# Kernel tuning notes

Measured on AMD Instinct MI355X. Metric: run time of the kernel, lower is better.

The kernel has to match this reference:

```python
import jax, jax.numpy as jnp
import numpy as np


def setup_inputs() -> dict:
    key = jax.random.key(0)
    k1, k2, k3 = jax.random.split(key, 3)
    B, M, T, D = 512, 4096, 48, 2
    preds = jax.random.normal(k1, (B, M), dtype=jnp.float32)
    target = jax.random.normal(k2, (B, 1, T, D), dtype=jnp.float32)
    memory = jax.random.normal(k3, (M, T, D), dtype=jnp.float32)
    return {"preds": preds, "target": target, "memory": memory}


def reference(preds, target, memory):
    # preds: [B, M]; target: [B, 1, T, D]; memory: [M, T, D]
    gt = target[:, 0]                                  # [B, T, D]
    diff = memory[None, :, :, :] - gt[:, None, :, :]   # [B, M, T, D]
    # mean over timesteps of per-timestep euclidean distance
    dist = jnp.sqrt(jnp.sum(diff * diff, axis=-1)).mean(axis=-1)  # [B, M]
    true_index = jnp.argmin(dist, axis=1)              # [B] int labels
    # cross-entropy of preds vs. nearest-mode labels, averaged over batch
    logp = jax.nn.log_softmax(preds, axis=1)           # [B, M]
    nll = -jnp.take_along_axis(logp, true_index[:, None], axis=1)[:, 0]  # [B]
    loss = nll.mean()
    return loss, true_index.astype(jnp.float32)
```

## Files before the change

kernel.cpp:

```cpp
#include <hip/hip_runtime.h>
#include <math.h>

#define B 512
#define M 4096
#define T 48
#define MCHUNK 8
#define NCH (M / MCHUNK)


__global__ __launch_bounds__(256) void k_transpose(const float* __restrict__ target,
                                                   float2* __restrict__ tgtT) {
    int i = blockIdx.x * 256 + threadIdx.x;
    int b = i / T, t = i - b * T;
    float2 v = ((const float2*)target)[i];
    tgtT[t * B + b] = v;
}

__global__ __launch_bounds__(256, 4) void k_dist(const float2* __restrict__ tgtT,
                                                 const float* __restrict__ memory,
                                                 unsigned long long* __restrict__ pval,
                                                 float* __restrict__ out0) {
    const int tid = threadIdx.x;
    const int b   = blockIdx.y * 256 + tid;
    const int ch  = blockIdx.x;
    const int m0  = ch * MCHUNK;

    if (ch == 0 && blockIdx.y == 0 && tid == 0) out0[0] = 0.0f;

    float acc[MCHUNK];
#pragma unroll
    for (int i = 0; i < MCHUNK; ++i) acc[i] = 0.f;

    for (int q = 0; q < T / 2; ++q) {
        float2 g0 = tgtT[(2 * q)     * B + b];
        float2 g1 = tgtT[(2 * q + 1) * B + b];
#pragma unroll
        for (int mi = 0; mi < MCHUNK; ++mi) {
            const float4* mr = (const float4*)(memory + (size_t)(m0 + mi) * (T * 2));
            float4 mv = mr[q];
            float dx0 = mv.x - g0.x, dy0 = mv.y - g0.y;
            float dx1 = mv.z - g1.x, dy1 = mv.w - g1.y;
            acc[mi] += __builtin_amdgcn_sqrtf(fmaf(dx0, dx0, dy0 * dy0));
            acc[mi] += __builtin_amdgcn_sqrtf(fmaf(dx1, dx1, dy1 * dy1));
        }
    }

    float bestv = INFINITY;
    int   besti = 0;
#pragma unroll
    for (int mi = 0; mi < MCHUNK; ++mi)
        if (acc[mi] < bestv) { bestv = acc[mi]; besti = m0 + mi; }

    pval[(size_t)b * NCH + ch] =
        ((unsigned long long)__float_as_uint(bestv) << 32) | (unsigned int)besti;
}

__global__ __launch_bounds__(256) void k_post(const float* __restrict__ preds,
                                              const unsigned long long* __restrict__ pval,
                                              float* __restrict__ out) {
    const int b   = blockIdx.x;
    const int tid = threadIdx.x;

    __shared__ unsigned long long sm[256];
    __shared__ float red[256];

    unsigned long long p0 = pval[(size_t)b * NCH + tid];
    unsigned long long p1 = pval[(size_t)b * NCH + 256 + tid];
    sm[tid] = p0 < p1 ? p0 : p1;
    __syncthreads();
    for (int s = 128; s > 0; s >>= 1) {
        if (tid < s) { unsigned long long o = sm[tid + s]; if (o < sm[tid]) sm[tid] = o; }
        __syncthreads();
    }
    const int idx = (int)(unsigned int)(sm[0] & 0xFFFFFFFFULL);
    __syncthreads();

    const float4* row = (const float4*)(preds + (size_t)b * M);
    float4 v[4];
    float mx = -INFINITY;
#pragma unroll
    for (int j = 0; j < 4; ++j) {
        v[j] = row[tid + j * 256];
        mx = fmaxf(mx, fmaxf(fmaxf(v[j].x, v[j].y), fmaxf(v[j].z, v[j].w)));
    }
    red[tid] = mx; __syncthreads();
    for (int s = 128; s > 0; s >>= 1) {
        if (tid < s) red[tid] = fmaxf(red[tid], red[tid + s]);
        __syncthreads();
    }
    mx = red[0];
    __syncthreads();

    float sum = 0.f;
#pragma unroll
    for (int j = 0; j < 4; ++j)
        sum += expf(v[j].x - mx) + expf(v[j].y - mx) + expf(v[j].z - mx) + expf(v[j].w - mx);
    red[tid] = sum; __syncthreads();
    for (int s = 128; s > 0; s >>= 1) {
        if (tid < s) red[tid] += red[tid + s];
        __syncthreads();
    }

    if (tid == 0) {
        float lse = mx + logf(red[0]);
        float nll = lse - preds[(size_t)b * M + idx];
        atomicAdd(out, nll * (1.0f / B));
        out[1 + b] = (float)idx;
    }
}

extern "C" void kernel_launch(void* const* d_in, const int* in_sizes, int n_in,
                              void* d_out, int out_size, void* d_ws, size_t ws_size,
                              hipStream_t stream) {
    const float* preds  = (const float*)d_in[0];
    const float* target = (const float*)d_in[1];
    const float* memory = (const float*)d_in[2];
    float* out = (float*)d_out;

    char* ws = (char*)d_ws;
    unsigned long long* pval = (unsigned long long*)ws;
    float2* tgtT = (float2*)(ws + (size_t)2 * 1024 * 1024);

    k_transpose<<<(B * T) / 256, 256, 0, stream>>>(target, tgtT);
    dim3 g1(NCH, B / 256);
    k_dist<<<g1, 256, 0, stream>>>(tgtT, memory, pval, out);
    k_post<<<B, 256, 0, stream>>>(preds, pval, out);
}
```

Baseline: 44.27 us.

## Stage memory rows in LDS, halve M chunk, warp-per-row post reduction

The distance kernel now handles 4 memory modes per block instead of 8, loads those modes' trajectories into shared memory once, and reads targets packed as float4 pairs of timesteps. Occupancy is raised through launch bounds. The post kernel gives each wavefront one batch row and reduces with shuffles instead of shared-memory tree reductions, and zeroing the loss moves into the prep kernel. The smaller chunk doubles the partial-argmin buffer and the number of blocks, which adds global write traffic and more work in the post reduction.

Result: slower. 47.11 us (+6.4%).

```diff
diff --git a/kernel.cpp b/kernel.cpp
--- a/kernel.cpp
+++ b/kernel.cpp
@@ -4,52 +4,72 @@
 #define B 512
 #define M 4096
 #define T 48
-#define MCHUNK 8
+#define MCHUNK 4
 #define NCH (M / MCHUNK)
 
 
-__global__ __launch_bounds__(256) void k_transpose(const float* __restrict__ target,
-                                                   float2* __restrict__ tgtT) {
+__global__ __launch_bounds__(256) void k_prep(const float* __restrict__ target,
+                                              float4* __restrict__ tgtP,
+                                              float* __restrict__ out0) {
     int i = blockIdx.x * 256 + threadIdx.x;
-    int b = i / T, t = i - b * T;
-    float2 v = ((const float2*)target)[i];
-    tgtT[t * B + b] = v;
+    if (i == 0) out0[0] = 0.0f;
+    int b = i / (T / 2), q = i - b * (T / 2);
+    float4 v = *(const float4*)(target + (size_t)b * (T * 2) + 4 * q);
+    tgtP[q * B + b] = v;
 }
 
-__global__ __launch_bounds__(256, 4) void k_dist(const float2* __restrict__ tgtT,
+__global__ __launch_bounds__(256, 8) void k_dist(const float4* __restrict__ tgtP,
                                                  const float* __restrict__ memory,
-                                                 unsigned long long* __restrict__ pval,
-                                                 float* __restrict__ out0) {
+                                                 unsigned long long* __restrict__ pval) {
     const int tid = threadIdx.x;
+    const int ch  = blockIdx.x;
     const int b   = blockIdx.y * 256 + tid;
-    const int ch  = blockIdx.x;
     const int m0  = ch * MCHUNK;
 
-    if (ch == 0 && blockIdx.y == 0 && tid == 0) out0[0] = 0.0f;
+    __shared__ float4 smem[MCHUNK * (T / 2)];
+    if (tid < MCHUNK * (T / 2))
+        smem[tid] = ((const float4*)(memory + (size_t)m0 * (T * 2)))[tid];
+    __syncthreads();
 
-    float acc[MCHUNK];
-#pragma unroll
-    for (int i = 0; i < MCHUNK; ++i) acc[i] = 0.f;
+    float acc0 = 0.f, acc1 = 0.f, acc2 = 0.f, acc3 = 0.f;
 
+#pragma unroll 6
     for (int q = 0; q < T / 2; ++q) {
-        float2 g0 = tgtT[(2 * q)     * B + b];
-        float2 g1 = tgtT[(2 * q + 1) * B + b];
-#pragma unroll
-        for (int mi = 0; mi < MCHUNK; ++mi) {
-            const float4* mr = (const float4*)(memory + (size_t)(m0 + mi) * (T * 2));
-            float4 mv = mr[q];
-            float dx0 = mv.x - g0.x, dy0 = mv.y - g0.y;
-            float dx1 = mv.z - g1.x, dy1 = mv.w - g1.y;
-            acc[mi] += __builtin_amdgcn_sqrtf(fmaf(dx0, dx0, dy0 * dy0));
-            acc[mi] += __builtin_amdgcn_sqrtf(fmaf(dx1, dx1, dy1 * dy1));
+        float4 g = tgtP[q * B + b];
+        {
+            float4 mv = smem[0 * (T / 2) + q];
+            float dx0 = mv.x - g.x, dy0 = mv.y - g.y;
+            float dx1 = mv.z - g.z, dy1 = mv.w - g.w;
+            acc0 += __builtin_amdgcn_sqrtf(fmaf(dx0, dx0, dy0 * dy0));
+            acc0 += __builtin_amdgcn_sqrtf(fmaf(dx1, dx1, dy1 * dy1));
+        }
+        {
+            float4 mv = smem[1 * (T / 2) + q];
+            float dx0 = mv.x - g.x, dy0 = mv.y - g.y;
+            float dx1 = mv.z - g.z, dy1 = mv.w - g.w;
+            acc1 += __builtin_amdgcn_sqrtf(fmaf(dx0, dx0, dy0 * dy0));
+            acc1 += __builtin_amdgcn_sqrtf(fmaf(dx1, dx1, dy1 * dy1));
+        }
+        {
+            float4 mv = smem[2 * (T / 2) + q];
+            float dx0 = mv.x - g.x, dy0 = mv.y - g.y;
+            float dx1 = mv.z - g.z, dy1 = mv.w - g.w;
+            acc2 += __builtin_amdgcn_sqrtf(fmaf(dx0, dx0, dy0 * dy0));
+            acc2 += __builtin_amdgcn_sqrtf(fmaf(dx1, dx1, dy1 * dy1));
+        }
+        {
+            float4 mv = smem[3 * (T / 2) + q];
+            float dx0 = mv.x - g.x, dy0 = mv.y - g.y;
+            float dx1 = mv.z - g.z, dy1 = mv.w - g.w;
+            acc3 += __builtin_amdgcn_sqrtf(fmaf(dx0, dx0, dy0 * dy0));
+            acc3 += __builtin_amdgcn_sqrtf(fmaf(dx1, dx1, dy1 * dy1));
         }
     }
 
-    float bestv = INFINITY;
-    int   besti = 0;
-#pragma unroll
-    for (int mi = 0; mi < MCHUNK; ++mi)
-        if (acc[mi] < bestv) { bestv = acc[mi]; besti = m0 + mi; }
+    float bestv = acc0; int besti = m0;
+    if (acc1 < bestv) { bestv = acc1; besti = m0 + 1; }
+    if (acc2 < bestv) { bestv = acc2; besti = m0 + 2; }
+    if (acc3 < bestv) { bestv = acc3; besti = m0 + 3; }
 
     pval[(size_t)b * NCH + ch] =
         ((unsigned long long)__float_as_uint(bestv) << 32) | (unsigned int)besti;
@@ -58,51 +78,45 @@
 __global__ __launch_bounds__(256) void k_post(const float* __restrict__ preds,
                                               const unsigned long long* __restrict__ pval,
                                               float* __restrict__ out) {
-    const int b   = blockIdx.x;
-    const int tid = threadIdx.x;
+    const int lane = threadIdx.x & 63;
+    const int wv   = threadIdx.x >> 6;
+    const int b    = blockIdx.x * 4 + wv;
 
-    __shared__ unsigned long long sm[256];
-    __shared__ float red[256];
-
-    unsigned long long p0 = pval[(size_t)b * NCH + tid];
-    unsigned long long p1 = pval[(size_t)b * NCH + 256 + tid];
-    sm[tid] = p0 < p1 ? p0 : p1;
-    __syncthreads();
-    for (int s = 128; s > 0; s >>= 1) {
-        if (tid < s) { unsigned long long o = sm[tid + s]; if (o < sm[tid]) sm[tid] = o; }
-        __syncthreads();
+    unsigned long long best = 0xFFFFFFFFFFFFFFFFULL;
+#pragma unroll
+    for (int j = 0; j < NCH / 64; ++j) {
+        unsigned long long p = pval[(size_t)b * NCH + j * 64 + lane];
+        if (p < best) best = p;
     }
-    const int idx = (int)(unsigned int)(sm[0] & 0xFFFFFFFFULL);
-    __syncthreads();
+#pragma unroll
+    for (int s = 32; s > 0; s >>= 1) {
+        unsigned long long o = __shfl_down(best, s);
+        if (o < best) best = o;
+    }
+    best = __shfl(best, 0);
+    const int idx = (int)(unsigned int)(best & 0xFFFFFFFFULL);
 
     const float4* row = (const float4*)(preds + (size_t)b * M);
-    float4 v[4];
+    float4 v[16];
     float mx = -INFINITY;
 #pragma unroll
-    for (int j = 0; j < 4; ++j) {
-        v[j] = row[tid + j * 256];
+    for (int j = 0; j < 16; ++j) {
+        v[j] = row[j * 64 + lane];
         mx = fmaxf(mx, fmaxf(fmaxf(v[j].x, v[j].y), fmaxf(v[j].z, v[j].w)));
     }
-    red[tid] = mx; __syncthreads();
-    for (int s = 128; s > 0; s >>= 1) {
-        if (tid < s) red[tid] = fmaxf(red[tid], red[tid + s]);
-        __syncthreads();
-    }
-    mx = red[0];
-    __syncthreads();
+#pragma unroll
+    for (int s = 32; s > 0; s >>= 1) mx = fmaxf(mx, __shfl_down(mx, s));
+    mx = __shfl(mx, 0);
 
     float sum = 0.f;
 #pragma unroll
-    for (int j = 0; j < 4; ++j)
+    for (int j = 0; j < 16; ++j)
         sum += expf(v[j].x - mx) + expf(v[j].y - mx) + expf(v[j].z - mx) + expf(v[j].w - mx);
-    red[tid] = sum; __syncthreads();
-    for (int s = 128; s > 0; s >>= 1) {
-        if (tid < s) red[tid] += red[tid + s];
-        __syncthreads();
-    }
+#pragma unroll
+    for (int s = 32; s > 0; s >>= 1) sum += __shfl_down(sum, s);
 
-    if (tid == 0) {
-        float lse = mx + logf(red[0]);
+    if (lane == 0) {
+        float lse = mx + logf(sum);
         float nll = lse - preds[(size_t)b * M + idx];
         atomicAdd(out, nll * (1.0f / B));
         out[1 + b] = (float)idx;
@@ -119,10 +133,10 @@
 
     char* ws = (char*)d_ws;
     unsigned long long* pval = (unsigned long long*)ws;
-    float2* tgtT = (float2*)(ws + (size_t)2 * 1024 * 1024);
+    float4* tgtP = (float4*)(ws + (size_t)4 * 1024 * 1024);
 
-    k_transpose<<<(B * T) / 256, 256, 0, stream>>>(target, tgtT);
+    k_prep<<<(B * T / 2) / 256, 256, 0, stream>>>(target, tgtP, out);
     dim3 g1(NCH, B / 256);
-    k_dist<<<g1, 256, 0, stream>>>(tgtT, memory, pval, out);
-    k_post<<<B, 256, 0, stream>>>(preds, pval, out);
+    k_dist<<<g1, 256, 0, stream>>>(tgtP, memory, pval);
+    k_post<<<B / 4, 256, 0, stream>>>(preds, pval, out);
 }
```

## Fuse transpose, distance and softmax-loss into one cooperative kernel

Applied to the files above, without the earlier changes.

Replaces the three kernel launches with a single cooperative kernel of 512 blocks that uses grid-wide syncs between the transpose, distance and post-processing phases. Each block now caches its memory chunk in shared memory and handles all 512 batch rows, two per thread. Partial argmins are stored transposed so the post phase can read them per batch. The aim is to remove launch gaps and repeated global loads of memory, at the cost of grid-sync overhead and the occupancy limits a cooperative launch imposes.

After: 148.2 us. +234.8%, slower.

```diff
diff --git a/kernel.cpp b/kernel.cpp
--- a/kernel.cpp
+++ b/kernel.cpp
@@ -1,5 +1,9 @@
 #include <hip/hip_runtime.h>
+#include <hip/hip_cooperative_groups.h>
 #include <math.h>
+
+namespace cg = cooperative_groups;
+typedef unsigned long long u64;
 
 #define B 512
 #define M 4096
@@ -8,104 +12,118 @@
 #define NCH (M / MCHUNK)
 
 
-__global__ __launch_bounds__(256) void k_transpose(const float* __restrict__ target,
-                                                   float2* __restrict__ tgtT) {
-    int i = blockIdx.x * 256 + threadIdx.x;
-    int b = i / T, t = i - b * T;
-    float2 v = ((const float2*)target)[i];
-    tgtT[t * B + b] = v;
-}
+__global__ __launch_bounds__(256, 2) void k_fused(const float* __restrict__ preds,
+                                                  const float* __restrict__ target,
+                                                  const float* __restrict__ memory,
+                                                  float* __restrict__ out,
+                                                  u64* __restrict__ pvalT,
+                                                  float4* __restrict__ tgtP) {
+    cg::grid_group grid = cg::this_grid();
+    const int tid = threadIdx.x;
+    const int bid = blockIdx.x;
 
-__global__ __launch_bounds__(256, 4) void k_dist(const float2* __restrict__ tgtT,
-                                                 const float* __restrict__ memory,
-                                                 unsigned long long* __restrict__ pval,
-                                                 float* __restrict__ out0) {
-    const int tid = threadIdx.x;
-    const int b   = blockIdx.y * 256 + tid;
-    const int ch  = blockIdx.x;
-    const int m0  = ch * MCHUNK;
+    __shared__ float4 smem[MCHUNK * (T / 2)];
+    __shared__ u64    smu[256];
+    __shared__ float  red[256];
 
-    if (ch == 0 && blockIdx.y == 0 && tid == 0) out0[0] = 0.0f;
+    {
+        int i = bid * 256 + tid;
+        if (i < B * (T / 2)) {
+            int b = i / (T / 2), q = i - b * (T / 2);
+            float4 v = *(const float4*)(target + (size_t)b * (T * 2) + 4 * q);
+            tgtP[q * B + b] = v;
+        }
+        if (i == 0) out[0] = 0.0f;
+    }
+    grid.sync();
 
-    float acc[MCHUNK];
+    {
+        const int ch = bid;
+        const int m0 = ch * MCHUNK;
+        if (tid < MCHUNK * (T / 2))
+            smem[tid] = ((const float4*)(memory + (size_t)m0 * (T * 2)))[tid];
+        __syncthreads();
+
+        float acc0[MCHUNK], acc1[MCHUNK];
 #pragma unroll
-    for (int i = 0; i < MCHUNK; ++i) acc[i] = 0.f;
+        for (int i = 0; i < MCHUNK; ++i) { acc0[i] = 0.f; acc1[i] = 0.f; }
 
-    for (int q = 0; q < T / 2; ++q) {
-        float2 g0 = tgtT[(2 * q)     * B + b];
-        float2 g1 = tgtT[(2 * q + 1) * B + b];
+#pragma unroll 4
+        for (int q = 0; q < T / 2; ++q) {
+            float4 g0 = tgtP[q * B + tid];
+            float4 g1 = tgtP[q * B + 256 + tid];
 #pragma unroll
-        for (int mi = 0; mi < MCHUNK; ++mi) {
-            const float4* mr = (const float4*)(memory + (size_t)(m0 + mi) * (T * 2));
-            float4 mv = mr[q];
-            float dx0 = mv.x - g0.x, dy0 = mv.y - g0.y;
-            float dx1 = mv.z - g1.x, dy1 = mv.w - g1.y;
-            acc[mi] += __builtin_amdgcn_sqrtf(fmaf(dx0, dx0, dy0 * dy0));
-            acc[mi] += __builtin_amdgcn_sqrtf(fmaf(dx1, dx1, dy1 * dy1));
+            for (int mi = 0; mi < MCHUNK; ++mi) {
+                float4 mv = smem[mi * (T / 2) + q];
+                float dx, dy;
+                dx = mv.x - g0.x; dy = mv.y - g0.y;
+                acc0[mi] += __builtin_amdgcn_sqrtf(fmaf(dx, dx, dy * dy));
+                dx = mv.z - g0.z; dy = mv.w - g0.w;
+                acc0[mi] += __builtin_amdgcn_sqrtf(fmaf(dx, dx, dy * dy));
+                dx = mv.x - g1.x; dy = mv.y - g1.y;
+                acc1[mi] += __builtin_amdgcn_sqrtf(fmaf(dx, dx, dy * dy));
+                dx = mv.z - g1.z; dy = mv.w - g1.w;
+                acc1[mi] += __builtin_amdgcn_sqrtf(fmaf(dx, dx, dy * dy));
+            }
         }
+
+        float bv0 = acc0[0]; int bi0 = m0;
+        float bv1 = acc1[0]; int bi1 = m0;
+#pragma unroll
+        for (int mi = 1; mi < MCHUNK; ++mi) {
+            if (acc0[mi] < bv0) { bv0 = acc0[mi]; bi0 = m0 + mi; }
+            if (acc1[mi] < bv1) { bv1 = acc1[mi]; bi1 = m0 + mi; }
+        }
+        pvalT[(size_t)ch * B + tid]       = ((u64)__float_as_uint(bv0) << 32) | (unsigned int)bi0;
+        pvalT[(size_t)ch * B + 256 + tid] = ((u64)__float_as_uint(bv1) << 32) | (unsigned int)bi1;
     }
+    grid.sync();
 
-    float bestv = INFINITY;
-    int   besti = 0;
+    {
+        const int b = bid;
+        u64 p0 = pvalT[(size_t)tid * B + b];
+        u64 p1 = pvalT[(size_t)(tid + 256) * B + b];
+        smu[tid] = p0 < p1 ? p0 : p1;
+        __syncthreads();
+        for (int s = 128; s > 0; s >>= 1) {
+            if (tid < s) { u64 o = smu[tid + s]; if (o < smu[tid]) smu[tid] = o; }
+            __syncthreads();
+        }
+        const int idx = (int)(unsigned int)(smu[0] & 0xFFFFFFFFULL);
+        __syncthreads();
+
+        const float4* row = (const float4*)(preds + (size_t)b * M);
+        float4 v[4];
+        float mx = -INFINITY;
 #pragma unroll
-    for (int mi = 0; mi < MCHUNK; ++mi)
-        if (acc[mi] < bestv) { bestv = acc[mi]; besti = m0 + mi; }
+        for (int j = 0; j < 4; ++j) {
+            v[j] = row[tid + j * 256];
+            mx = fmaxf(mx, fmaxf(fmaxf(v[j].x, v[j].y), fmaxf(v[j].z, v[j].w)));
+        }
+        red[tid] = mx; __syncthreads();
+        for (int s = 128; s > 0; s >>= 1) {
+            if (tid < s) red[tid] = fmaxf(red[tid], red[tid + s]);
+            __syncthreads();
+        }
+        mx = red[0];
+        __syncthreads();
 
-    pval[(size_t)b * NCH + ch] =
-        ((unsigned long long)__float_as_uint(bestv) << 32) | (unsigned int)besti;
-}
+        float sum = 0.f;
+#pragma unroll
+        for (int j = 0; j < 4; ++j)
+            sum += expf(v[j].x - mx) + expf(v[j].y - mx) + expf(v[j].z - mx) + expf(v[j].w - mx);
+        red[tid] = sum; __syncthreads();
+        for (int s = 128; s > 0; s >>= 1) {
+            if (tid < s) red[tid] += red[tid + s];
+            __syncthreads();
+        }
 
-__global__ __launch_bounds__(256) void k_post(const float* __restrict__ preds,
-                                              const unsigned long long* __restrict__ pval,
-                                              float* __restrict__ out) {
-    const int b   = blockIdx.x;
-    const int tid = threadIdx.x;
-
-    __shared__ unsigned long long sm[256];
-    __shared__ float red[256];
-
-    unsigned long long p0 = pval[(size_t)b * NCH + tid];
-    unsigned long long p1 = pval[(size_t)b * NCH + 256 + tid];
-    sm[tid] = p0 < p1 ? p0 : p1;
-    __syncthreads();
-    for (int s = 128; s > 0; s >>= 1) {
-        if (tid < s) { unsigned long long o = sm[tid + s]; if (o < sm[tid]) sm[tid] = o; }
-        __syncthreads();
-    }
-    const int idx = (int)(unsigned int)(sm[0] & 0xFFFFFFFFULL);
-    __syncthreads();
-
-    const float4* row = (const float4*)(preds + (size_t)b * M);
-    float4 v[4];
-    float mx = -INFINITY;
-#pragma unroll
-    for (int j = 0; j < 4; ++j) {
-        v[j] = row[tid + j * 256];
-        mx = fmaxf(mx, fmaxf(fmaxf(v[j].x, v[j].y), fmaxf(v[j].z, v[j].w)));
-    }
-    red[tid] = mx; __syncthreads();
-    for (int s = 128; s > 0; s >>= 1) {
-        if (tid < s) red[tid] = fmaxf(red[tid], red[tid + s]);
-        __syncthreads();
-    }
-    mx = red[0];
-    __syncthreads();
-
-    float sum = 0.f;
-#pragma unroll
-    for (int j = 0; j < 4; ++j)
-        sum += expf(v[j].x - mx) + expf(v[j].y - mx) + expf(v[j].z - mx) + expf(v[j].w - mx);
-    red[tid] = sum; __syncthreads();
-    for (int s = 128; s > 0; s >>= 1) {
-        if (tid < s) red[tid] += red[tid + s];
-        __syncthreads();
-    }
-
-    if (tid == 0) {
-        float lse = mx + logf(red[0]);
-        float nll = lse - preds[(size_t)b * M + idx];
-        atomicAdd(out, nll * (1.0f / B));
-        out[1 + b] = (float)idx;
+        if (tid == 0) {
+            float lse = mx + logf(red[0]);
+            float nll = lse - preds[(size_t)b * M + idx];
+            atomicAdd(out, nll * (1.0f / B));
+            out[1 + b] = (float)idx;
+        }
     }
 }
 
@@ -118,11 +136,11 @@
     float* out = (float*)d_out;
 
     char* ws = (char*)d_ws;
-    unsigned long long* pval = (unsigned long long*)ws;
-    float2* tgtT = (float2*)(ws + (size_t)2 * 1024 * 1024);
+    u64* pvalT   = (u64*)ws;
+    float4* tgtP = (float4*)(ws + (size_t)2 * 1024 * 1024);
 
-    k_transpose<<<(B * T) / 256, 256, 0, stream>>>(target, tgtT);
-    dim3 g1(NCH, B / 256);
-    k_dist<<<g1, 256, 0, stream>>>(tgtT, memory, pval, out);
-    k_post<<<B, 256, 0, stream>>>(preds, pval, out);
+    void* args[] = {(void*)&preds, (void*)&target, (void*)&memory,
+                    (void*)&out, (void*)&pvalT, (void*)&tgtP};
+    hipLaunchCooperativeKernel((const void*)k_fused, dim3(NCH), dim3(256),
+                               args, 0, stream);
 }
```

## Transpose memory instead of target and tile batch rows in shared memory

Applied to the files above, without the earlier changes.

The distance kernel is reorganised so each thread owns one memory mode and loops over a tile of 8 batch rows kept in shared memory, reading a transposed memory array with coalesced loads. Before, each thread owned one batch row and read uniform memory rows. Per-block argmin now uses wavefront shuffles, and the post kernel reduces only 16 partials per row. This cuts the partial-result traffic and the reduction work, but adds a larger transpose of the 4096x48 memory array and shared-memory reads in the inner loop.

Result: slower. 45.28 us (+2.3%).

```diff
diff --git a/kernel.cpp b/kernel.cpp
--- a/kernel.cpp
+++ b/kernel.cpp
@@ -1,79 +1,91 @@
 #include <hip/hip_runtime.h>
 #include <math.h>
+
+typedef unsigned long long u64;
 
 #define B 512
 #define M 4096
 #define T 48
-#define MCHUNK 8
-#define NCH (M / MCHUNK)
+#define BTILE 8
+#define MBLK 256
+#define NMB (M / MBLK)
 
 
-__global__ __launch_bounds__(256) void k_transpose(const float* __restrict__ target,
-                                                   float2* __restrict__ tgtT) {
+__global__ __launch_bounds__(256) void k_trans(const float* __restrict__ memory,
+                                               float2* __restrict__ memT,
+                                               float* __restrict__ out0) {
     int i = blockIdx.x * 256 + threadIdx.x;
-    int b = i / T, t = i - b * T;
-    float2 v = ((const float2*)target)[i];
-    tgtT[t * B + b] = v;
+    if (i == 0) out0[0] = 0.0f;
+    int m = i / T, t = i - m * T;
+    memT[t * M + m] = ((const float2*)memory)[i];
 }
 
-__global__ __launch_bounds__(256, 4) void k_dist(const float2* __restrict__ tgtT,
-                                                 const float* __restrict__ memory,
-                                                 unsigned long long* __restrict__ pval,
-                                                 float* __restrict__ out0) {
+__global__ __launch_bounds__(256) void k_dist(const float* __restrict__ target,
+                                              const float2* __restrict__ memT,
+                                              u64* __restrict__ pval) {
     const int tid = threadIdx.x;
-    const int b   = blockIdx.y * 256 + tid;
-    const int ch  = blockIdx.x;
-    const int m0  = ch * MCHUNK;
+    const int m   = blockIdx.x * MBLK + tid;
+    const int b0  = blockIdx.y * BTILE;
 
-    if (ch == 0 && blockIdx.y == 0 && tid == 0) out0[0] = 0.0f;
+    __shared__ float tg[BTILE * T * 2];
+    __shared__ u64   su[4][BTILE];
 
-    float acc[MCHUNK];
+    if (tid < BTILE * T * 2 / 4)
+        ((float4*)tg)[tid] = ((const float4*)(target + (size_t)b0 * (T * 2)))[tid];
+    __syncthreads();
+
+    float acc[BTILE];
 #pragma unroll
-    for (int i = 0; i < MCHUNK; ++i) acc[i] = 0.f;
+    for (int bi = 0; bi < BTILE; ++bi) acc[bi] = 0.f;
 
-    for (int q = 0; q < T / 2; ++q) {
-        float2 g0 = tgtT[(2 * q)     * B + b];
-        float2 g1 = tgtT[(2 * q + 1) * B + b];
+#pragma unroll 2
+    for (int t = 0; t < T; ++t) {
+        float2 mv = memT[t * M + m];
 #pragma unroll
-        for (int mi = 0; mi < MCHUNK; ++mi) {
-            const float4* mr = (const float4*)(memory + (size_t)(m0 + mi) * (T * 2));
-            float4 mv = mr[q];
-            float dx0 = mv.x - g0.x, dy0 = mv.y - g0.y;
-            float dx1 = mv.z - g1.x, dy1 = mv.w - g1.y;
-            acc[mi] += __builtin_amdgcn_sqrtf(fmaf(dx0, dx0, dy0 * dy0));
-            acc[mi] += __builtin_amdgcn_sqrtf(fmaf(dx1, dx1, dy1 * dy1));
+        for (int bi = 0; bi < BTILE; ++bi) {
+            float dx = mv.x - tg[bi * (T * 2) + 2 * t];
+            float dy = mv.y - tg[bi * (T * 2) + 2 * t + 1];
+            acc[bi] += __builtin_amdgcn_sqrtf(fmaf(dx, dx, dy * dy));
         }
     }
 
-    float bestv = INFINITY;
-    int   besti = 0;
+    const int lane = tid & 63, wv = tid >> 6;
 #pragma unroll
-    for (int mi = 0; mi < MCHUNK; ++mi)
-        if (acc[mi] < bestv) { bestv = acc[mi]; besti = m0 + mi; }
-
-    pval[(size_t)b * NCH + ch] =
-        ((unsigned long long)__float_as_uint(bestv) << 32) | (unsigned int)besti;
+    for (int bi = 0; bi < BTILE; ++bi) {
+        u64 p = ((u64)__float_as_uint(acc[bi]) << 32) | (unsigned int)m;
+#pragma unroll
+        for (int s = 32; s > 0; s >>= 1) {
+            u64 o = __shfl_down(p, s);
+            if (o < p) p = o;
+        }
+        if (lane == 0) su[wv][bi] = p;
+    }
+    __syncthreads();
+    if (tid < BTILE) {
+        u64 p = su[0][tid];
+        if (su[1][tid] < p) p = su[1][tid];
+        if (su[2][tid] < p) p = su[2][tid];
+        if (su[3][tid] < p) p = su[3][tid];
+        pval[(size_t)(b0 + tid) * NMB + blockIdx.x] = p;
+    }
 }
 
 __global__ __launch_bounds__(256) void k_post(const float* __restrict__ preds,
-                                              const unsigned long long* __restrict__ pval,
+                                              const u64* __restrict__ pval,
                                               float* __restrict__ out) {
-    const int b   = blockIdx.x;
-    const int tid = threadIdx.x;
+    const int b = blockIdx.x, tid = threadIdx.x;
+    __shared__ float red[256];
+    __shared__ int   sidx;
 
-    __shared__ unsigned long long sm[256];
-    __shared__ float red[256];
-
-    unsigned long long p0 = pval[(size_t)b * NCH + tid];
-    unsigned long long p1 = pval[(size_t)b * NCH + 256 + tid];
-    sm[tid] = p0 < p1 ? p0 : p1;
-    __syncthreads();
-    for (int s = 128; s > 0; s >>= 1) {
-        if (tid < s) { unsigned long long o = sm[tid + s]; if (o < sm[tid]) sm[tid] = o; }
-        __syncthreads();
+    if (tid < 64) {
+        u64 p = (tid < NMB) ? pval[(size_t)b * NMB + tid] : 0xFFFFFFFFFFFFFFFFULL;
+#pragma unroll
+        for (int s = 8; s > 0; s >>= 1) {
+            u64 o = __shfl_down(p, s);
+            if (o < p) p = o;
+        }
+        if (tid == 0) sidx = (int)(unsigned int)(p & 0xFFFFFFFFULL);
     }
-    const int idx = (int)(unsigned int)(sm[0] & 0xFFFFFFFFULL);
-    __syncthreads();
 
     const float4* row = (const float4*)(preds + (size_t)b * M);
     float4 v[4];
@@ -103,9 +115,9 @@
 
     if (tid == 0) {
         float lse = mx + logf(red[0]);
-        float nll = lse - preds[(size_t)b * M + idx];
+        float nll = lse - preds[(size_t)b * M + sidx];
         atomicAdd(out, nll * (1.0f / B));
-        out[1 + b] = (float)idx;
+        out[1 + b] = (float)sidx;
     }
 }
 
@@ -118,11 +130,11 @@
     float* out = (float*)d_out;
 
     char* ws = (char*)d_ws;
-    unsigned long long* pval = (unsigned long long*)ws;
-    float2* tgtT = (float2*)(ws + (size_t)2 * 1024 * 1024);
+    u64* pval    = (u64*)ws;
+    float2* memT = (float2*)(ws + 64 * 1024);
 
-    k_transpose<<<(B * T) / 256, 256, 0, stream>>>(target, tgtT);
-    dim3 g1(NCH, B / 256);
-    k_dist<<<g1, 256, 0, stream>>>(tgtT, memory, pval, out);
+    k_trans<<<(M * T) / 256, 256, 0, stream>>>(memory, memT, out);
+    dim3 g1(NMB, B / BTILE);
+    k_dist<<<g1, 256, 0, stream>>>(target, memT, pval);
     k_post<<<B, 256, 0, stream>>>(preds, pval, out);
 }
```
